# Optimization experiments

Measured on AMD Instinct MI355X. Metric: run time of the kernel, lower is better.

## Reference

```python
import jax, jax.numpy as jnp
import numpy as np

B_G = 16        # number of point clouds
N_PER = 32768   # points per cloud (equal -> no padding)
T = B_G * N_PER
CIN = 16
D = 32          # global_dim
H = 4           # num_heads
HD = D // H
L = 2           # layers
EPS_LN = 1e-5
EPS_Z = 1e-6


def setup_inputs() -> dict:
    key = jax.random.key(0)
    ks = jax.random.split(key, 32)
    r = lambda i, shape, s: (jax.random.normal(ks[i], shape, dtype=jnp.float32) * s)
    inp = {
        "x": r(0, (T, CIN), 1.0),
        "pos": r(1, (T, 3), 1.0),
        "batch": (jnp.arange(T, dtype=jnp.int32) // N_PER),
        "w_in": r(2, (CIN, D), CIN ** -0.5),
        "b_in": r(3, (D,), 0.02),
        "w_pos": r(4, (3, D), 3 ** -0.5),
        "b_pos": r(5, (D,), 0.02),
        "wq": r(6, (L, D, D), D ** -0.5),
        "bq": r(7, (L, D), 0.02),
        "wk": r(8, (L, D, D), D ** -0.5),
        "bk": r(9, (L, D), 0.02),
        "wv": r(10, (L, D, D), D ** -0.5),
        "bv": r(11, (L, D), 0.02),
        "wo": r(12, (L, D, D), D ** -0.5),
        "bo": r(13, (L, D), 0.02),
        "g1": jnp.ones((L, D), jnp.float32),
        "be1": jnp.zeros((L, D), jnp.float32),
        "w1": r(14, (L, D, 2 * D), D ** -0.5),
        "bf1": r(15, (L, 2 * D), 0.02),
        "w2": r(16, (L, 2 * D, D), (2 * D) ** -0.5),
        "bf2": r(17, (L, D), 0.02),
        "g2": jnp.ones((L, D), jnp.float32),
        "be2": jnp.zeros((L, D), jnp.float32),
    }
    return inp


def _layernorm(h, g, b):
    mu = jnp.mean(h, axis=-1, keepdims=True)
    var = jnp.mean(jnp.square(h - mu), axis=-1, keepdims=True)
    return (h - mu) * jax.lax.rsqrt(var + EPS_LN) * g + b


def _linear_attn(h, wq, bq, wk, bk, wv, bv, wo, bo):
    B, N, C = h.shape
    def heads(w, b):
        return (h @ w + b).reshape(B, N, H, HD).transpose(0, 2, 1, 3)  # [B,H,N,hd]
    q = jax.nn.elu(heads(wq, bq)) + 1.0   # ELU feature map phi(.)
    k = jax.nn.elu(heads(wk, bk)) + 1.0
    v = heads(wv, bv)
    kv = jnp.einsum("bhnd,bhne->bhde", k, v)            # O(N) KV summary
    ksum = k.sum(axis=2)                                   # [B,H,hd]
    z = 1.0 / (jnp.einsum("bhnd,bhd->bhn", q, ksum) + EPS_Z)
    out = jnp.einsum("bhnd,bhde->bhne", q, kv) * z[..., None]
    out = out.transpose(0, 2, 1, 3).reshape(B, N, C)
    return out @ wo + bo


def reference(x, pos, batch, w_in, b_in, w_pos, b_pos, wq, bq, wk, bk, wv, bv,
              wo, bo, g1, be1, w1, bf1, w2, bf2, g2, be2):
    # to_dense_batch: batch is sorted; compute per-point index within its segment
    counts = jax.ops.segment_sum(jnp.ones((T,), jnp.int32), batch, num_segments=B_G)
    starts = jnp.concatenate([jnp.zeros((1,), jnp.int32), jnp.cumsum(counts)[:-1]])
    idx = jnp.arange(T, dtype=jnp.int32) - starts[batch]
    x_dense = jnp.zeros((B_G, N_PER, CIN), x.dtype).at[batch, idx].set(x)
    pos_dense = jnp.zeros((B_G, N_PER, 3), pos.dtype).at[batch, idx].set(pos)

    h = (x_dense @ w_in + b_in) + (pos_dense @ w_pos + b_pos)  # [B,N,D]
    for l in range(L):
        h = _layernorm(h + _linear_attn(h, wq[l], bq[l], wk[l], bk[l],
                                        wv[l], bv[l], wo[l], bo[l]), g1[l], be1[l])
        ffn = jax.nn.relu(h @ w1[l] + bf1[l]) @ w2[l] + bf2[l]
        h = _layernorm(h + ffn, g2[l], be2[l])
    return h[batch, idx]  # back to [T, D] (h[mask])
```

## Files before the change

### kernel.cpp

```cpp
#include <hip/hip_runtime.h>

#define KVSZ 288
#define EPS_LN 1e-5f
#define EPS_Z  1e-6f

typedef __attribute__((ext_vector_type(8))) short bf16x8;
typedef __attribute__((ext_vector_type(4))) float f32x4;

#define MFMA(a, b, c) __builtin_amdgcn_mfma_f32_16x16x32_bf16(a, b, c, 0, 0, 0)

#define WQ  0
#define WO  1024
#define KVM 2048
#define W1  3072
#define W2  5120
#define WKN 7168
#define WVN 8192

__device__ __forceinline__ unsigned short f2bf(float f) {
  union { float f; unsigned u; } x; x.f = f;
  unsigned r = x.u + 0x7fff + ((x.u >> 16) & 1);
  return (unsigned short)(r >> 16);
}

__device__ __forceinline__ unsigned pkbf(float a, float b) {
#if __has_builtin(__builtin_amdgcn_cvt_pk_bf16_f32)
  typedef __attribute__((ext_vector_type(2))) __bf16 bf16x2_t;
  bf16x2_t v = __builtin_amdgcn_cvt_pk_bf16_f32(a, b);
  return __builtin_bit_cast(unsigned, v);
#else
  return (unsigned)f2bf(a) | ((unsigned)f2bf(b) << 16);
#endif
}

__device__ __forceinline__ void lds_fence() { asm volatile("s_waitcnt lgkmcnt(0)" ::: "memory"); }
__device__ __forceinline__ float phi(float x) { return x > 0.f ? x + 1.f : __expf(x); }

__device__ __forceinline__ int perm32(int kp) {
  return ((kp & 4) << 2) | (((kp >> 3) << 2) + (kp & 3));
}

__device__ __forceinline__ bf16x8 bbuild(f32x4 lo, f32x4 hi) {
  union { bf16x8 v; unsigned u[4]; } cv;
  cv.u[0] = pkbf(lo[0], lo[1]); cv.u[1] = pkbf(lo[2], lo[3]);
  cv.u[2] = pkbf(hi[0], hi[1]); cv.u[3] = pkbf(hi[2], hi[3]);
  return cv.v;
}

__device__ __forceinline__ void stage_a32(unsigned short* dst, const float* __restrict__ W,
                                          int N, int tid) {
  for (int i = tid; i < 32 * N; i += 256) {
    int n = i >> 5, kp = i & 31;
    dst[i] = f2bf(W[perm32(kp) * N + n]);
  }
}
__device__ __forceinline__ void stage_a64(unsigned short* dst, const float* __restrict__ W,
                                          int tid) {
  for (int i = tid; i < 64 * 32; i += 256) {
    int n = i >> 6, kp = i & 63;
    int kl = ((kp >> 5) << 5) + perm32(kp & 31);
    dst[i] = f2bf(W[kl * 32 + n]);
  }
}
__device__ __forceinline__ void stage_kvm_t(unsigned short* dst, const float* __restrict__ kvg,
                                            int tid) {
  for (int i = tid; i < 1024; i += 256) {
    int e = i >> 5, kp = i & 31;
    int d = perm32(kp);
    float v = ((d >> 3) == (e >> 3)) ? kvg[(e >> 3) * 64 + (d & 7) * 8 + (e & 7)] : 0.f;
    dst[i] = f2bf(v);
  }
}

__device__ __forceinline__ void ln_t(f32x4& a0, f32x4& a1, float4 g0, float4 g1,
                                     float4 b0, float4 b1) {
  float s = a0[0] + a0[1] + a0[2] + a0[3] + a1[0] + a1[1] + a1[2] + a1[3];
  s += __shfl_xor(s, 16); s += __shfl_xor(s, 32);
  float mu = s * (1.f / 32.f);
  float vv = 0.f;
#pragma unroll
  for (int r = 0; r < 4; r++) {
    a0[r] -= mu; a1[r] -= mu;
    vv += a0[r] * a0[r] + a1[r] * a1[r];
  }
  vv += __shfl_xor(vv, 16); vv += __shfl_xor(vv, 32);
  float rstd = rsqrtf(vv * (1.f / 32.f) + EPS_LN);
  a0[0] = a0[0] * rstd * g0.x + b0.x; a0[1] = a0[1] * rstd * g0.y + b0.y;
  a0[2] = a0[2] * rstd * g0.z + b0.z; a0[3] = a0[3] * rstd * g0.w + b0.w;
  a1[0] = a1[0] * rstd * g1.x + b1.x; a1[1] = a1[1] * rstd * g1.y + b1.y;
  a1[2] = a1[2] * rstd * g1.z + b1.z; a1[3] = a1[3] * rstd * g1.w + b1.w;
}

__device__ __forceinline__ void layer_core_t(
    f32x4* hc0, f32x4* hc1, const unsigned short* ws, int quad, int m,
    const float* __restrict__ bq, const float* __restrict__ bo,
    const float* __restrict__ g1, const float* __restrict__ be1,
    const float* __restrict__ bf1, const float* __restrict__ bf2,
    const float* __restrict__ g2, const float* __restrict__ be2,
    const float* __restrict__ kvg) {
  const int k0 = quad * 8, q4 = quad * 4;
  {
    const bf16x8 wqA0 = *(const bf16x8*)(ws + WQ + m * 32 + k0);
    const bf16x8 wqA1 = *(const bf16x8*)(ws + WQ + (16 + m) * 32 + k0);
    const bf16x8 kvA0 = *(const bf16x8*)(ws + KVM + m * 32 + k0);
    const bf16x8 kvA1 = *(const bf16x8*)(ws + KVM + (16 + m) * 32 + k0);
    const bf16x8 woA0 = *(const bf16x8*)(ws + WO + m * 32 + k0);
    const bf16x8 woA1 = *(const bf16x8*)(ws + WO + (16 + m) * 32 + k0);
    const float4 bq0 = *(const float4*)(bq + q4), bq1 = *(const float4*)(bq + 16 + q4);
    const float4 bo0 = *(const float4*)(bo + q4), bo1 = *(const float4*)(bo + 16 + q4);
    const float4 g10 = *(const float4*)(g1 + q4), g11 = *(const float4*)(g1 + 16 + q4);
    const float4 e10 = *(const float4*)(be1 + q4), e11 = *(const float4*)(be1 + 16 + q4);
    const float4 ks0 = *(const float4*)(kvg + 256 + q4);
    const float4 ks1 = *(const float4*)(kvg + 272 + q4);
#pragma unroll
    for (int mt = 0; mt < 4; mt++) {
      bf16x8 hB = bbuild(hc0[mt], hc1[mt]);
      f32x4 q0 = {bq0.x, bq0.y, bq0.z, bq0.w};
      f32x4 q1 = {bq1.x, bq1.y, bq1.z, bq1.w};
      q0 = MFMA(wqA0, hB, q0);
      q1 = MFMA(wqA1, hB, q1);
#pragma unroll
      for (int r = 0; r < 4; r++) { q0[r] = phi(q0[r]); q1[r] = phi(q1[r]); }
      bf16x8 qB = bbuild(q0, q1);
      f32x4 zz = {0.f, 0.f, 0.f, 0.f};
      f32x4 at0 = MFMA(kvA0, qB, zz);
      f32x4 at1 = MFMA(kvA1, qB, zz);
      float p0 = q0[0] * ks0.x + q0[1] * ks0.y + q0[2] * ks0.z + q0[3] * ks0.w;
      float p1 = q1[0] * ks1.x + q1[1] * ks1.y + q1[2] * ks1.z + q1[3] * ks1.w;
      p0 += __shfl_xor(p0, 16);
      p1 += __shfl_xor(p1, 16);
      float z0 = 1.f / (p0 + EPS_Z), z1 = 1.f / (p1 + EPS_Z);
      bf16x8 aB;
      {
        union { bf16x8 v; unsigned u[4]; } cv;
        cv.u[0] = pkbf(at0[0] * z0, at0[1] * z0); cv.u[1] = pkbf(at0[2] * z0, at0[3] * z0);
        cv.u[2] = pkbf(at1[0] * z1, at1[1] * z1); cv.u[3] = pkbf(at1[2] * z1, at1[3] * z1);
        aB = cv.v;
      }
      f32x4 h0 = hc0[mt], h1 = hc1[mt];
      h0[0] += bo0.x; h0[1] += bo0.y; h0[2] += bo0.z; h0[3] += bo0.w;
      h1[0] += bo1.x; h1[1] += bo1.y; h1[2] += bo1.z; h1[3] += bo1.w;
      h0 = MFMA(woA0, aB, h0);
      h1 = MFMA(woA1, aB, h1);
      ln_t(h0, h1, g10, g11, e10, e11);
      hc0[mt] = h0; hc1[mt] = h1;
    }
  }
  {
    bf16x8 w1A[4]; float4 b1f[4];
#pragma unroll
    for (int nt = 0; nt < 4; nt++) {
      w1A[nt] = *(const bf16x8*)(ws + W1 + (nt * 16 + m) * 32 + k0);
      b1f[nt] = *(const float4*)(bf1 + nt * 16 + q4);
    }
    const bf16x8 w2L0 = *(const bf16x8*)(ws + W2 + m * 64 + k0);
    const bf16x8 w2H0 = *(const bf16x8*)(ws + W2 + m * 64 + 32 + k0);
    const bf16x8 w2L1 = *(const bf16x8*)(ws + W2 + (16 + m) * 64 + k0);
    const bf16x8 w2H1 = *(const bf16x8*)(ws + W2 + (16 + m) * 64 + 32 + k0);
    const float4 b20 = *(const float4*)(bf2 + q4), b21 = *(const float4*)(bf2 + 16 + q4);
    const float4 g20 = *(const float4*)(g2 + q4), g21 = *(const float4*)(g2 + 16 + q4);
    const float4 e20 = *(const float4*)(be2 + q4), e21 = *(const float4*)(be2 + 16 + q4);
#pragma unroll
    for (int mt = 0; mt < 4; mt++) {
      bf16x8 hB = bbuild(hc0[mt], hc1[mt]);
      f32x4 hd[4];
#pragma unroll
      for (int nt = 0; nt < 4; nt++) {
        f32x4 ini = {b1f[nt].x, b1f[nt].y, b1f[nt].z, b1f[nt].w};
        hd[nt] = MFMA(w1A[nt], hB, ini);
#pragma unroll
        for (int r = 0; r < 4; r++) hd[nt][r] = fmaxf(hd[nt][r], 0.f);
      }
      bf16x8 fL = bbuild(hd[0], hd[1]);
      bf16x8 fH = bbuild(hd[2], hd[3]);
      f32x4 o0 = hc0[mt], o1 = hc1[mt];
      o0[0] += b20.x; o0[1] += b20.y; o0[2] += b20.z; o0[3] += b20.w;
      o1[0] += b21.x; o1[1] += b21.y; o1[2] += b21.z; o1[3] += b21.w;
      o0 = MFMA(w2L0, fL, o0);
      o0 = MFMA(w2H0, fH, o0);
      o1 = MFMA(w2L1, fL, o1);
      o1 = MFMA(w2H1, fH, o1);
      ln_t(o0, o1, g20, g21, e20, e21);
      hc0[mt] = o0; hc1[mt] = o1;
    }
  }
}

__device__ __forceinline__ void kv_stage_t(
    const f32x4* hc0, const f32x4* hc1, unsigned short* tw, const unsigned short* ws,
    int offk, int offv, float* blk, int quad, int m,
    const float* __restrict__ bk, const float* __restrict__ bv) {
  const int k0 = quad * 8, q4 = quad * 4;
  unsigned short* Tk = tw;
  unsigned short* Tv = tw + 1280;
  const bf16x8 wkA0 = *(const bf16x8*)(ws + offk + m * 32 + k0);
  const bf16x8 wkA1 = *(const bf16x8*)(ws + offk + (16 + m) * 32 + k0);
  const bf16x8 wvA0 = *(const bf16x8*)(ws + offv + m * 32 + k0);
  const bf16x8 wvA1 = *(const bf16x8*)(ws + offv + (16 + m) * 32 + k0);
  const float4 bk0 = *(const float4*)(bk + q4), bk1 = *(const float4*)(bk + 16 + q4);
  const float4 bv0 = *(const float4*)(bv + q4), bv1 = *(const float4*)(bv + 16 + q4);
  f32x4 accA = {0.f, 0.f, 0.f, 0.f}, accB = {0.f, 0.f, 0.f, 0.f};
  f32x4 ksa0 = {0.f, 0.f, 0.f, 0.f}, ksa1 = {0.f, 0.f, 0.f, 0.f};
#pragma unroll
  for (int ch = 0; ch < 2; ch++) {
#pragma unroll
    for (int mtl = 0; mtl < 2; mtl++) {
      int mt = ch * 2 + mtl;
      bf16x8 hB = bbuild(hc0[mt], hc1[mt]);
      f32x4 kn0 = {bk0.x, bk0.y, bk0.z, bk0.w};
      f32x4 kn1 = {bk1.x, bk1.y, bk1.z, bk1.w};
      f32x4 vn0 = {bv0.x, bv0.y, bv0.z, bv0.w};
      f32x4 vn1 = {bv1.x, bv1.y, bv1.z, bv1.w};
      kn0 = MFMA(wkA0, hB, kn0);
      kn1 = MFMA(wkA1, hB, kn1);
      vn0 = MFMA(wvA0, hB, vn0);
      vn1 = MFMA(wvA1, hB, vn1);
      int cb = mtl * 16 + m;
#pragma unroll
      for (int r = 0; r < 4; r++) {
        kn0[r] = phi(kn0[r]); kn1[r] = phi(kn1[r]);
        ksa0[r] += kn0[r];    ksa1[r] += kn1[r];
        Tk[(q4 + r) * 40 + cb]      = f2bf(kn0[r]);
        Tk[(16 + q4 + r) * 40 + cb] = f2bf(kn1[r]);
        Tv[(q4 + r) * 40 + cb]      = f2bf(vn0[r]);
        Tv[(16 + q4 + r) * 40 + cb] = f2bf(vn1[r]);
      }
    }
    lds_fence();
    bf16x8 akL = *(const bf16x8*)(Tk + m * 40 + k0);
    bf16x8 akH = *(const bf16x8*)(Tk + (16 + m) * 40 + k0);
    bf16x8 avL = *(const bf16x8*)(Tv + m * 40 + k0);
    bf16x8 avH = *(const bf16x8*)(Tv + (16 + m) * 40 + k0);
    accA = MFMA(akL, avL, accA);
    accB = MFMA(akH, avH, accB);
    lds_fence();
  }
#pragma unroll
  for (int r = 0; r < 4; r++) {
    float v0 = ksa0[r], v1 = ksa1[r];
    v0 += __shfl_xor(v0, 1); v0 += __shfl_xor(v0, 2); v0 += __shfl_xor(v0, 4); v0 += __shfl_xor(v0, 8);
    v1 += __shfl_xor(v1, 1); v1 += __shfl_xor(v1, 2); v1 += __shfl_xor(v1, 4); v1 += __shfl_xor(v1, 8);
    if (m == 0) {
      atomicAdd(&blk[256 + q4 + r], v0);
      atomicAdd(&blk[272 + q4 + r], v1);
    }
  }
  if ((quad >> 1) == (m >> 3)) {
    int h0 = quad >> 1, h1 = 2 + (quad >> 1), e = m & 7;
#pragma unroll
    for (int r = 0; r < 4; r++) {
      int d = (q4 + r) & 7;
      atomicAdd(&blk[h0 * 64 + d * 8 + e], accA[r]);
      atomicAdd(&blk[h1 * 64 + d * 8 + e], accB[r]);
    }
  }
}

__global__ __launch_bounds__(256) void k_embed(
    const float* __restrict__ x, const float* __restrict__ pos,
    const float* __restrict__ w_in, const float* __restrict__ b_in,
    const float* __restrict__ w_pos, const float* __restrict__ b_pos,
    const float* __restrict__ wk, const float* __restrict__ bk,
    const float* __restrict__ wv, const float* __restrict__ bv,
    float* __restrict__ hout, float* __restrict__ gkv) {
  __shared__ __align__(16) unsigned short ws[3072];
  __shared__ __align__(16) unsigned short tiles[4 * 2560];
  __shared__ float blk[KVSZ];
  const int tid = threadIdx.x;
  const int wv_ = tid >> 6, lane = tid & 63, quad = lane >> 4, m = lane & 15;
  unsigned short* tw = tiles + wv_ * 2560;
  for (int i = tid; i < 1024; i += 256) {
    int n = i >> 5, k = i & 31;
    float v = k < 16 ? w_in[k * 32 + n] : (k < 19 ? w_pos[(k - 16) * 32 + n] : 0.f);
    ws[i] = f2bf(v);
  }
  stage_a32(ws + 1024, wk, 32, tid);
  stage_a32(ws + 2048, wv, 32, tid);
  for (int i = tid; i < KVSZ; i += 256) blk[i] = 0.f;
  __syncthreads();
  const int wbase = blockIdx.x * 256 + wv_ * 64;
  const int cloud = blockIdx.x >> 7;
  const int k0 = quad * 8, q4 = quad * 4;
  const bf16x8 weA0 = *(const bf16x8*)(ws + m * 32 + k0);
  const bf16x8 weA1 = *(const bf16x8*)(ws + (16 + m) * 32 + k0);
  float4 bi0, bi1;
  {
    float4 a = *(const float4*)(b_in + q4), b = *(const float4*)(b_pos + q4);
    bi0 = make_float4(a.x + b.x, a.y + b.y, a.z + b.z, a.w + b.w);
    float4 c = *(const float4*)(b_in + 16 + q4), d = *(const float4*)(b_pos + 16 + q4);
    bi1 = make_float4(c.x + d.x, c.y + d.y, c.z + d.z, c.w + d.w);
  }
  f32x4 hc0[4], hc1[4];
#pragma unroll
  for (int mt = 0; mt < 4; mt++) {
    int p = wbase + mt * 16 + m;
    union { bf16x8 v; unsigned u[4]; } xb;
    xb.u[0] = xb.u[1] = xb.u[2] = xb.u[3] = 0;
    if (quad < 2) {
      const float4* xp = (const float4*)(x + (size_t)p * 16 + quad * 8);
      float4 t0 = xp[0], t1 = xp[1];
      xb.u[0] = pkbf(t0.x, t0.y); xb.u[1] = pkbf(t0.z, t0.w);
      xb.u[2] = pkbf(t1.x, t1.y); xb.u[3] = pkbf(t1.z, t1.w);
    } else if (quad == 2) {
      const float* pp = pos + (size_t)p * 3;
      xb.u[0] = pkbf(pp[0], pp[1]); xb.u[1] = pkbf(pp[2], 0.f);
    }
    f32x4 i0 = {bi0.x, bi0.y, bi0.z, bi0.w};
    f32x4 i1 = {bi1.x, bi1.y, bi1.z, bi1.w};
    hc0[mt] = MFMA(weA0, xb.v, i0);
    hc1[mt] = MFMA(weA1, xb.v, i1);
    float* hp = hout + (size_t)p * 32;
    *(float4*)(hp + q4)      = make_float4(hc0[mt][0], hc0[mt][1], hc0[mt][2], hc0[mt][3]);
    *(float4*)(hp + 16 + q4) = make_float4(hc1[mt][0], hc1[mt][1], hc1[mt][2], hc1[mt][3]);
  }
  kv_stage_t(hc0, hc1, tw, ws, 1024, 2048, blk, quad, m, bk, bv);
  __syncthreads();
  float* g = gkv + cloud * KVSZ;
  for (int i = tid; i < KVSZ; i += 256) atomicAdd(&g[i], blk[i]);
}

__global__ __launch_bounds__(256) void k_mid(
    const float* __restrict__ wq, const float* __restrict__ bq,
    const float* __restrict__ wo, const float* __restrict__ bo,
    const float* __restrict__ g1, const float* __restrict__ be1,
    const float* __restrict__ w1, const float* __restrict__ bf1,
    const float* __restrict__ w2, const float* __restrict__ bf2,
    const float* __restrict__ g2, const float* __restrict__ be2,
    const float* __restrict__ wkn, const float* __restrict__ bkn,
    const float* __restrict__ wvn, const float* __restrict__ bvn,
    const float* __restrict__ kv_in, float* __restrict__ gkv_out,
    float* __restrict__ hbuf) {
  __shared__ __align__(16) unsigned short ws[9216];
  __shared__ __align__(16) unsigned short tiles[4 * 2560];
  __shared__ float blk[KVSZ];
  const int tid = threadIdx.x;
  const int wv_ = tid >> 6, lane = tid & 63, quad = lane >> 4, m = lane & 15;
  unsigned short* tw = tiles + wv_ * 2560;
  const int cloud = blockIdx.x >> 7;
  stage_a32(ws + WQ, wq, 32, tid);
  stage_a32(ws + WO, wo, 32, tid);
  stage_kvm_t(ws + KVM, kv_in + cloud * KVSZ, tid);
  stage_a32(ws + W1, w1, 64, tid);
  stage_a64(ws + W2, w2, tid);
  stage_a32(ws + WKN, wkn, 32, tid);
  stage_a32(ws + WVN, wvn, 32, tid);
  for (int i = tid; i < KVSZ; i += 256) blk[i] = 0.f;
  __syncthreads();
  const int wbase = blockIdx.x * 256 + wv_ * 64;
  const int q4 = quad * 4;
  f32x4 hc0[4], hc1[4];
#pragma unroll
  for (int mt = 0; mt < 4; mt++) {
    const float* hp = hbuf + (size_t)(wbase + mt * 16 + m) * 32;
    float4 lo = *(const float4*)(hp + q4);
    float4 hi = *(const float4*)(hp + 16 + q4);
    hc0[mt][0] = lo.x; hc0[mt][1] = lo.y; hc0[mt][2] = lo.z; hc0[mt][3] = lo.w;
    hc1[mt][0] = hi.x; hc1[mt][1] = hi.y; hc1[mt][2] = hi.z; hc1[mt][3] = hi.w;
  }
  layer_core_t(hc0, hc1, ws, quad, m, bq, bo, g1, be1, bf1, bf2, g2, be2,
               kv_in + cloud * KVSZ);
#pragma unroll
  for (int mt = 0; mt < 4; mt++) {
    float* hp = hbuf + (size_t)(wbase + mt * 16 + m) * 32;
    *(float4*)(hp + q4)      = make_float4(hc0[mt][0], hc0[mt][1], hc0[mt][2], hc0[mt][3]);
    *(float4*)(hp + 16 + q4) = make_float4(hc1[mt][0], hc1[mt][1], hc1[mt][2], hc1[mt][3]);
  }
  kv_stage_t(hc0, hc1, tw, ws, WKN, WVN, blk, quad, m, bkn, bvn);
  __syncthreads();
  float* g = gkv_out + cloud * KVSZ;
  for (int i = tid; i < KVSZ; i += 256) atomicAdd(&g[i], blk[i]);
}

__global__ __launch_bounds__(256) void k_last(
    const float* __restrict__ wq, const float* __restrict__ bq,
    const float* __restrict__ wo, const float* __restrict__ bo,
    const float* __restrict__ g1, const float* __restrict__ be1,
    const float* __restrict__ w1, const float* __restrict__ bf1,
    const float* __restrict__ w2, const float* __restrict__ bf2,
    const float* __restrict__ g2, const float* __restrict__ be2,
    const float* __restrict__ kv_in, float* __restrict__ hbuf) {
  __shared__ __align__(16) unsigned short ws[7168];
  const int tid = threadIdx.x;
  const int wv_ = tid >> 6, lane = tid & 63, quad = lane >> 4, m = lane & 15;
  const int cloud = blockIdx.x >> 7;
  stage_a32(ws + WQ, wq, 32, tid);
  stage_a32(ws + WO, wo, 32, tid);
  stage_kvm_t(ws + KVM, kv_in + cloud * KVSZ, tid);
  stage_a32(ws + W1, w1, 64, tid);
  stage_a64(ws + W2, w2, tid);
  __syncthreads();
  const int wbase = blockIdx.x * 256 + wv_ * 64;
  const int q4 = quad * 4;
  f32x4 hc0[4], hc1[4];
#pragma unroll
  for (int mt = 0; mt < 4; mt++) {
    const float* hp = hbuf + (size_t)(wbase + mt * 16 + m) * 32;
    float4 lo = *(const float4*)(hp + q4);
    float4 hi = *(const float4*)(hp + 16 + q4);
    hc0[mt][0] = lo.x; hc0[mt][1] = lo.y; hc0[mt][2] = lo.z; hc0[mt][3] = lo.w;
    hc1[mt][0] = hi.x; hc1[mt][1] = hi.y; hc1[mt][2] = hi.z; hc1[mt][3] = hi.w;
  }
  layer_core_t(hc0, hc1, ws, quad, m, bq, bo, g1, be1, bf1, bf2, g2, be2,
               kv_in + cloud * KVSZ);
#pragma unroll
  for (int mt = 0; mt < 4; mt++) {
    float* hp = hbuf + (size_t)(wbase + mt * 16 + m) * 32;
    *(float4*)(hp + q4)      = make_float4(hc0[mt][0], hc0[mt][1], hc0[mt][2], hc0[mt][3]);
    *(float4*)(hp + 16 + q4) = make_float4(hc1[mt][0], hc1[mt][1], hc1[mt][2], hc1[mt][3]);
  }
}

extern "C" void kernel_launch(void* const* d_in, const int* in_sizes, int n_in,
                              void* d_out, int out_size, void* d_ws, size_t ws_size,
                              hipStream_t stream) {
  (void)in_sizes; (void)n_in; (void)out_size; (void)ws_size;
  const float* x     = (const float*)d_in[0];
  const float* pos   = (const float*)d_in[1];
  const float* w_in  = (const float*)d_in[3];
  const float* b_in  = (const float*)d_in[4];
  const float* w_pos = (const float*)d_in[5];
  const float* b_pos = (const float*)d_in[6];
  const float* wq  = (const float*)d_in[7];
  const float* bq  = (const float*)d_in[8];
  const float* wk  = (const float*)d_in[9];
  const float* bk  = (const float*)d_in[10];
  const float* wv  = (const float*)d_in[11];
  const float* bv  = (const float*)d_in[12];
  const float* wo  = (const float*)d_in[13];
  const float* bo  = (const float*)d_in[14];
  const float* g1  = (const float*)d_in[15];
  const float* be1 = (const float*)d_in[16];
  const float* w1  = (const float*)d_in[17];
  const float* bf1 = (const float*)d_in[18];
  const float* w2  = (const float*)d_in[19];
  const float* bf2 = (const float*)d_in[20];
  const float* g2  = (const float*)d_in[21];
  const float* be2 = (const float*)d_in[22];
  float* out   = (float*)d_out;
  float* kvbuf = (float*)d_ws;

  hipMemsetAsync(kvbuf, 0, 2 * 16 * KVSZ * sizeof(float), stream);
  dim3 grid(2048), block(256);
  k_embed<<<grid, block, 0, stream>>>(x, pos, w_in, b_in, w_pos, b_pos,
                                      wk, bk, wv, bv, out, kvbuf);
  k_mid<<<grid, block, 0, stream>>>(wq, bq, wo, bo, g1, be1, w1, bf1, w2, bf2, g2, be2,
                                    wk + 1024, bk + 32, wv + 1024, bv + 32,
                                    kvbuf, kvbuf + 16 * KVSZ, out);
  k_last<<<grid, block, 0, stream>>>(wq + 1024, bq + 32, wo + 1024, bo + 32,
                                     g1 + 32, be1 + 32, w1 + 2048, bf1 + 64,
                                     w2 + 2048, bf2 + 32, g2 + 32, be2 + 32,
                                     kvbuf + 16 * KVSZ, out);
}
```

Measured before the change: 306.9 us.

## Prepack bf16 weights once, build KV matrix in registers, store activations as bf16

A single-block prep kernel now converts and permutes all weights to bf16 in workspace once. The main kernels read these A-fragments straight from global memory, so they no longer redo per-block LDS staging and its barrier. The block-diagonal KV matrix is assembled per lane in registers instead of in LDS. When the workspace is large enough, the intermediate hidden state between kernels is kept in bf16 instead of fp32, halving that traffic at some cost in precision. The trade-off is an extra serial launch and global-memory weight reads.

```diff
diff --git a/kernel.cpp b/kernel.cpp
--- a/kernel.cpp
+++ b/kernel.cpp
@@ -9,13 +9,14 @@
 
 #define MFMA(a, b, c) __builtin_amdgcn_mfma_f32_16x16x32_bf16(a, b, c, 0, 0, 0)
 
-#define WQ  0
-#define WO  1024
-#define KVM 2048
-#define W1  3072
-#define W2  5120
-#define WKN 7168
-#define WVN 8192
+#define PWE 0
+#define LBASE(l) (1024 + (l) * 8192)
+#define PQ 0
+#define PO 1024
+#define P1 2048
+#define P2 4096
+#define PK 6144
+#define PV 7168
 
 __device__ __forceinline__ unsigned short f2bf(float f) {
   union { float f; unsigned u; } x; x.f = f;
@@ -33,6 +34,10 @@
 #endif
 }
 
+__device__ __forceinline__ float bfu(unsigned short s) {
+  union { float f; unsigned u; } x; x.u = ((unsigned)s) << 16; return x.f;
+}
+
 __device__ __forceinline__ void lds_fence() { asm volatile("s_waitcnt lgkmcnt(0)" ::: "memory"); }
 __device__ __forceinline__ float phi(float x) { return x > 0.f ? x + 1.f : __expf(x); }
 
@@ -62,14 +67,23 @@
     dst[i] = f2bf(W[kl * 32 + n]);
   }
 }
-__device__ __forceinline__ void stage_kvm_t(unsigned short* dst, const float* __restrict__ kvg,
-                                            int tid) {
-  for (int i = tid; i < 1024; i += 256) {
-    int e = i >> 5, kp = i & 31;
-    int d = perm32(kp);
-    float v = ((d >> 3) == (e >> 3)) ? kvg[(e >> 3) * 64 + (d & 7) * 8 + (e & 7)] : 0.f;
-    dst[i] = f2bf(v);
-  }
+
+__device__ __forceinline__ void make_kvm(bf16x8& A0, bf16x8& A1,
+                                         const float* __restrict__ kvg,
+                                         int quad, int m) {
+  union { bf16x8 v; unsigned short s[8]; unsigned u[4]; } a, b;
+  a.u[0] = a.u[1] = a.u[2] = a.u[3] = 0u;
+  b.u[0] = b.u[1] = b.u[2] = b.u[3] = 0u;
+  if ((quad >> 1) == (m >> 3)) {
+    int h0 = m >> 3, e7 = m & 7, dq = (quad & 1) * 4;
+    const float* p0 = kvg + h0 * 64 + dq * 8 + e7;
+    const float* p1 = kvg + (2 + h0) * 64 + dq * 8 + e7;
+    a.s[0] = f2bf(p0[0]);  a.s[1] = f2bf(p0[8]);
+    a.s[2] = f2bf(p0[16]); a.s[3] = f2bf(p0[24]);
+    b.s[4] = f2bf(p1[0]);  b.s[5] = f2bf(p1[8]);
+    b.s[6] = f2bf(p1[16]); b.s[7] = f2bf(p1[24]);
+  }
+  A0 = a.v; A1 = b.v;
 }
 
 __device__ __forceinline__ void ln_t(f32x4& a0, f32x4& a1, float4 g0, float4 g1,
@@ -91,21 +105,21 @@
   a1[2] = a1[2] * rstd * g1.z + b1.z; a1[3] = a1[3] * rstd * g1.w + b1.w;
 }
 
-__device__ __forceinline__ void layer_core_t(
-    f32x4* hc0, f32x4* hc1, const unsigned short* ws, int quad, int m,
+__device__ __forceinline__ void layer_core_g(
+    f32x4 (&hc0)[4], f32x4 (&hc1)[4], const unsigned short* __restrict__ pwl,
+    const float* __restrict__ kvg, int quad, int m,
     const float* __restrict__ bq, const float* __restrict__ bo,
     const float* __restrict__ g1, const float* __restrict__ be1,
     const float* __restrict__ bf1, const float* __restrict__ bf2,
-    const float* __restrict__ g2, const float* __restrict__ be2,
-    const float* __restrict__ kvg) {
+    const float* __restrict__ g2, const float* __restrict__ be2) {
   const int k0 = quad * 8, q4 = quad * 4;
   {
-    const bf16x8 wqA0 = *(const bf16x8*)(ws + WQ + m * 32 + k0);
-    const bf16x8 wqA1 = *(const bf16x8*)(ws + WQ + (16 + m) * 32 + k0);
-    const bf16x8 kvA0 = *(const bf16x8*)(ws + KVM + m * 32 + k0);
-    const bf16x8 kvA1 = *(const bf16x8*)(ws + KVM + (16 + m) * 32 + k0);
-    const bf16x8 woA0 = *(const bf16x8*)(ws + WO + m * 32 + k0);
-    const bf16x8 woA1 = *(const bf16x8*)(ws + WO + (16 + m) * 32 + k0);
+    const bf16x8 wqA0 = *(const bf16x8*)(pwl + PQ + m * 32 + k0);
+    const bf16x8 wqA1 = *(const bf16x8*)(pwl + PQ + (16 + m) * 32 + k0);
+    const bf16x8 woA0 = *(const bf16x8*)(pwl + PO + m * 32 + k0);
+    const bf16x8 woA1 = *(const bf16x8*)(pwl + PO + (16 + m) * 32 + k0);
+    bf16x8 kvA0, kvA1;
+    make_kvm(kvA0, kvA1, kvg, quad, m);
     const float4 bq0 = *(const float4*)(bq + q4), bq1 = *(const float4*)(bq + 16 + q4);
     const float4 bo0 = *(const float4*)(bo + q4), bo1 = *(const float4*)(bo + 16 + q4);
     const float4 g10 = *(const float4*)(g1 + q4), g11 = *(const float4*)(g1 + 16 + q4);
@@ -150,13 +164,13 @@
     bf16x8 w1A[4]; float4 b1f[4];
 #pragma unroll
     for (int nt = 0; nt < 4; nt++) {
-      w1A[nt] = *(const bf16x8*)(ws + W1 + (nt * 16 + m) * 32 + k0);
+      w1A[nt] = *(const bf16x8*)(pwl + P1 + (nt * 16 + m) * 32 + k0);
       b1f[nt] = *(const float4*)(bf1 + nt * 16 + q4);
     }
-    const bf16x8 w2L0 = *(const bf16x8*)(ws + W2 + m * 64 + k0);
-    const bf16x8 w2H0 = *(const bf16x8*)(ws + W2 + m * 64 + 32 + k0);
-    const bf16x8 w2L1 = *(const bf16x8*)(ws + W2 + (16 + m) * 64 + k0);
-    const bf16x8 w2H1 = *(const bf16x8*)(ws + W2 + (16 + m) * 64 + 32 + k0);
+    const bf16x8 w2L0 = *(const bf16x8*)(pwl + P2 + m * 64 + k0);
+    const bf16x8 w2H0 = *(const bf16x8*)(pwl + P2 + m * 64 + 32 + k0);
+    const bf16x8 w2L1 = *(const bf16x8*)(pwl + P2 + (16 + m) * 64 + k0);
+    const bf16x8 w2H1 = *(const bf16x8*)(pwl + P2 + (16 + m) * 64 + 32 + k0);
     const float4 b20 = *(const float4*)(bf2 + q4), b21 = *(const float4*)(bf2 + 16 + q4);
     const float4 g20 = *(const float4*)(g2 + q4), g21 = *(const float4*)(g2 + 16 + q4);
     const float4 e20 = *(const float4*)(be2 + q4), e21 = *(const float4*)(be2 + 16 + q4);
@@ -186,17 +200,18 @@
   }
 }
 
-__device__ __forceinline__ void kv_stage_t(
-    const f32x4* hc0, const f32x4* hc1, unsigned short* tw, const unsigned short* ws,
-    int offk, int offv, float* blk, int quad, int m,
+__device__ __forceinline__ void kv_stage_g(
+    const f32x4 (&hc0)[4], const f32x4 (&hc1)[4], unsigned short* tw,
+    const unsigned short* __restrict__ pwk, const unsigned short* __restrict__ pwv,
+    float* blk, int quad, int m,
     const float* __restrict__ bk, const float* __restrict__ bv) {
   const int k0 = quad * 8, q4 = quad * 4;
   unsigned short* Tk = tw;
   unsigned short* Tv = tw + 1280;
-  const bf16x8 wkA0 = *(const bf16x8*)(ws + offk + m * 32 + k0);
-  const bf16x8 wkA1 = *(const bf16x8*)(ws + offk + (16 + m) * 32 + k0);
-  const bf16x8 wvA0 = *(const bf16x8*)(ws + offv + m * 32 + k0);
-  const bf16x8 wvA1 = *(const bf16x8*)(ws + offv + (16 + m) * 32 + k0);
+  const bf16x8 wkA0 = *(const bf16x8*)(pwk + m * 32 + k0);
+  const bf16x8 wkA1 = *(const bf16x8*)(pwk + (16 + m) * 32 + k0);
+  const bf16x8 wvA0 = *(const bf16x8*)(pwv + m * 32 + k0);
+  const bf16x8 wvA1 = *(const bf16x8*)(pwv + (16 + m) * 32 + k0);
   const float4 bk0 = *(const float4*)(bk + q4), bk1 = *(const float4*)(bk + 16 + q4);
   const float4 bv0 = *(const float4*)(bv + q4), bv1 = *(const float4*)(bv + 16 + q4);
   f32x4 accA = {0.f, 0.f, 0.f, 0.f}, accB = {0.f, 0.f, 0.f, 0.f};
@@ -256,33 +271,48 @@
   }
 }
 
+__global__ __launch_bounds__(256) void k_prep(
+    const float* __restrict__ w_in, const float* __restrict__ w_pos,
+    const float* __restrict__ wq, const float* __restrict__ wk,
+    const float* __restrict__ wv, const float* __restrict__ wo,
+    const float* __restrict__ w1, const float* __restrict__ w2,
+    unsigned short* __restrict__ pw) {
+  const int tid = threadIdx.x;
+  for (int i = tid; i < 1024; i += 256) {
+    int n = i >> 5, k = i & 31;
+    float v = k < 16 ? w_in[k * 32 + n] : (k < 19 ? w_pos[(k - 16) * 32 + n] : 0.f);
+    pw[PWE + i] = f2bf(v);
+  }
+  for (int l = 0; l < 2; l++) {
+    unsigned short* b = pw + LBASE(l);
+    stage_a32(b + PQ, wq + l * 1024, 32, tid);
+    stage_a32(b + PO, wo + l * 1024, 32, tid);
+    stage_a32(b + P1, w1 + l * 2048, 64, tid);
+    stage_a64(b + P2, w2 + l * 2048, tid);
+    stage_a32(b + PK, wk + l * 1024, 32, tid);
+    stage_a32(b + PV, wv + l * 1024, 32, tid);
+  }
+}
+
+template <int H16>
 __global__ __launch_bounds__(256) void k_embed(
     const float* __restrict__ x, const float* __restrict__ pos,
-    const float* __restrict__ w_in, const float* __restrict__ b_in,
-    const float* __restrict__ w_pos, const float* __restrict__ b_pos,
-    const float* __restrict__ wk, const float* __restrict__ bk,
-    const float* __restrict__ wv, const float* __restrict__ bv,
-    float* __restrict__ hout, float* __restrict__ gkv) {
-  __shared__ __align__(16) unsigned short ws[3072];
+    const float* __restrict__ b_in, const float* __restrict__ b_pos,
+    const float* __restrict__ bk, const float* __restrict__ bv,
+    const unsigned short* __restrict__ pw, unsigned short* __restrict__ hb,
+    float* __restrict__ hf, float* __restrict__ gkv) {
   __shared__ __align__(16) unsigned short tiles[4 * 2560];
   __shared__ float blk[KVSZ];
   const int tid = threadIdx.x;
   const int wv_ = tid >> 6, lane = tid & 63, quad = lane >> 4, m = lane & 15;
   unsigned short* tw = tiles + wv_ * 2560;
-  for (int i = tid; i < 1024; i += 256) {
-    int n = i >> 5, k = i & 31;
-    float v = k < 16 ? w_in[k * 32 + n] : (k < 19 ? w_pos[(k - 16) * 32 + n] : 0.f);
-    ws[i] = f2bf(v);
-  }
-  stage_a32(ws + 1024, wk, 32, tid);
-  stage_a32(ws + 2048, wv, 32, tid);
+  const int cloud = blockIdx.x >> 7;
+  const int wbase = blockIdx.x * 256 + wv_ * 64;
+  const int k0 = quad * 8, q4 = quad * 4;
   for (int i = tid; i < KVSZ; i += 256) blk[i] = 0.f;
   __syncthreads();
-  const int wbase = blockIdx.x * 256 + wv_ * 64;
-  const int cloud = blockIdx.x >> 7;
-  const int k0 = quad * 8, q4 = quad * 4;
-  const bf16x8 weA0 = *(const bf16x8*)(ws + m * 32 + k0);
-  const bf16x8 weA1 = *(const bf16x8*)(ws + (16 + m) * 32 + k0);
+  const bf16x8 weA0 = *(const bf16x8*)(pw + PWE + m * 32 + k0);
+  const bf16x8 weA1 = *(const bf16x8*)(pw + PWE + (16 + m) * 32 + k0);
   float4 bi0, bi1;
   {
     float4 a = *(const float4*)(b_in + q4), b = *(const float4*)(b_pos + q4);
@@ -309,102 +339,117 @@
     f32x4 i1 = {bi1.x, bi1.y, bi1.z, bi1.w};
     hc0[mt] = MFMA(weA0, xb.v, i0);
     hc1[mt] = MFMA(weA1, xb.v, i1);
-    float* hp = hout + (size_t)p * 32;
-    *(float4*)(hp + q4)      = make_float4(hc0[mt][0], hc0[mt][1], hc0[mt][2], hc0[mt][3]);
-    *(float4*)(hp + 16 + q4) = make_float4(hc1[mt][0], hc1[mt][1], hc1[mt][2], hc1[mt][3]);
-  }
-  kv_stage_t(hc0, hc1, tw, ws, 1024, 2048, blk, quad, m, bk, bv);
+    if (H16) {
+      *(bf16x8*)(hb + ((size_t)p * 32 + quad * 8)) = bbuild(hc0[mt], hc1[mt]);
+    } else {
+      float* hp = hf + (size_t)p * 32;
+      *(float4*)(hp + q4)      = make_float4(hc0[mt][0], hc0[mt][1], hc0[mt][2], hc0[mt][3]);
+      *(float4*)(hp + 16 + q4) = make_float4(hc1[mt][0], hc1[mt][1], hc1[mt][2], hc1[mt][3]);
+    }
+  }
+  kv_stage_g(hc0, hc1, tw, pw + LBASE(0) + PK, pw + LBASE(0) + PV, blk, quad, m, bk, bv);
   __syncthreads();
   float* g = gkv + cloud * KVSZ;
   for (int i = tid; i < KVSZ; i += 256) atomicAdd(&g[i], blk[i]);
 }
 
+template <int H16>
 __global__ __launch_bounds__(256) void k_mid(
-    const float* __restrict__ wq, const float* __restrict__ bq,
-    const float* __restrict__ wo, const float* __restrict__ bo,
+    const float* __restrict__ bq, const float* __restrict__ bo,
     const float* __restrict__ g1, const float* __restrict__ be1,
-    const float* __restrict__ w1, const float* __restrict__ bf1,
-    const float* __restrict__ w2, const float* __restrict__ bf2,
+    const float* __restrict__ bf1, const float* __restrict__ bf2,
     const float* __restrict__ g2, const float* __restrict__ be2,
-    const float* __restrict__ wkn, const float* __restrict__ bkn,
-    const float* __restrict__ wvn, const float* __restrict__ bvn,
-    const float* __restrict__ kv_in, float* __restrict__ gkv_out,
-    float* __restrict__ hbuf) {
-  __shared__ __align__(16) unsigned short ws[9216];
+    const float* __restrict__ bkn, const float* __restrict__ bvn,
+    const unsigned short* __restrict__ pw, const float* __restrict__ kv_in,
+    float* __restrict__ gkv_out, unsigned short* __restrict__ hb,
+    float* __restrict__ hf) {
   __shared__ __align__(16) unsigned short tiles[4 * 2560];
   __shared__ float blk[KVSZ];
   const int tid = threadIdx.x;
   const int wv_ = tid >> 6, lane = tid & 63, quad = lane >> 4, m = lane & 15;
   unsigned short* tw = tiles + wv_ * 2560;
   const int cloud = blockIdx.x >> 7;
-  stage_a32(ws + WQ, wq, 32, tid);
-  stage_a32(ws + WO, wo, 32, tid);
-  stage_kvm_t(ws + KVM, kv_in + cloud * KVSZ, tid);
-  stage_a32(ws + W1, w1, 64, tid);
-  stage_a64(ws + W2, w2, tid);
-  stage_a32(ws + WKN, wkn, 32, tid);
-  stage_a32(ws + WVN, wvn, 32, tid);
+  const int wbase = blockIdx.x * 256 + wv_ * 64;
+  const int q4 = quad * 4;
   for (int i = tid; i < KVSZ; i += 256) blk[i] = 0.f;
   __syncthreads();
+  f32x4 hc0[4], hc1[4];
+#pragma unroll
+  for (int mt = 0; mt < 4; mt++) {
+    int p = wbase + mt * 16 + m;
+    if (H16) {
+      bf16x8 hv = *(const bf16x8*)(hb + ((size_t)p * 32 + quad * 8));
+#pragma unroll
+      for (int r = 0; r < 4; r++) {
+        hc0[mt][r] = bfu((unsigned short)hv[r]);
+        hc1[mt][r] = bfu((unsigned short)hv[4 + r]);
+      }
+    } else {
+      const float* hp = hf + (size_t)p * 32;
+      float4 lo = *(const float4*)(hp + q4);
+      float4 hi = *(const float4*)(hp + 16 + q4);
+      hc0[mt][0] = lo.x; hc0[mt][1] = lo.y; hc0[mt][2] = lo.z; hc0[mt][3] = lo.w;
+      hc1[mt][0] = hi.x; hc1[mt][1] = hi.y; hc1[mt][2] = hi.z; hc1[mt][3] = hi.w;
+    }
+  }
+  layer_core_g(hc0, hc1, pw + LBASE(0), kv_in + cloud * KVSZ, quad, m,
+               bq, bo, g1, be1, bf1, bf2, g2, be2);
+#pragma unroll
+  for (int mt = 0; mt < 4; mt++) {
+    int p = wbase + mt * 16 + m;
+    if (H16) {
+      *(bf16x8*)(hb + ((size_t)p * 32 + quad * 8)) = bbuild(hc0[mt], hc1[mt]);
+    } else {
+      float* hp = hf + (size_t)p * 32;
+      *(float4*)(hp + q4)      = make_float4(hc0[mt][0], hc0[mt][1], hc0[mt][2], hc0[mt][3]);
+      *(float4*)(hp + 16 + q4) = make_float4(hc1[mt][0], hc1[mt][1], hc1[mt][2], hc1[mt][3]);
+    }
+  }
+  kv_stage_g(hc0, hc1, tw, pw + LBASE(1) + PK, pw + LBASE(1) + PV, blk, quad, m,
+             bkn, bvn);
+  __syncthreads();
+  float* g = gkv_out + cloud * KVSZ;
+  for (int i = tid; i < KVSZ; i += 256) atomicAdd(&g[i], blk[i]);
+}
+
+template <int H16>
+__global__ __launch_bounds__(256) void k_last(
+    const float* __restrict__ bq, const float* __restrict__ bo,
+    const float* __restrict__ g1, const float* __restrict__ be1,
+    const float* __restrict__ bf1, const float* __restrict__ bf2,
+    const float* __restrict__ g2, const float* __restrict__ be2,
+    const unsigned short* __restrict__ pw, const float* __restrict__ kv_in,
+    const unsigned short* __restrict__ hb, float* __restrict__ out) {
+  const int tid = threadIdx.x;
+  const int wv_ = tid >> 6, lane = tid & 63, quad = lane >> 4, m = lane & 15;
+  const int cloud = blockIdx.x >> 7;
   const int wbase = blockIdx.x * 256 + wv_ * 64;
   const int q4 = quad * 4;
   f32x4 hc0[4], hc1[4];
 #pragma unroll
   for (int mt = 0; mt < 4; mt++) {
-    const float* hp = hbuf + (size_t)(wbase + mt * 16 + m) * 32;
-    float4 lo = *(const float4*)(hp + q4);
-    float4 hi = *(const float4*)(hp + 16 + q4);
-    hc0[mt][0] = lo.x; hc0[mt][1] = lo.y; hc0[mt][2] = lo.z; hc0[mt][3] = lo.w;
-    hc1[mt][0] = hi.x; hc1[mt][1] = hi.y; hc1[mt][2] = hi.z; hc1[mt][3] = hi.w;
-  }
-  layer_core_t(hc0, hc1, ws, quad, m, bq, bo, g1, be1, bf1, bf2, g2, be2,
-               kv_in + cloud * KVSZ);
+    int p = wbase + mt * 16 + m;
+    if (H16) {
+      bf16x8 hv = *(const bf16x8*)(hb + ((size_t)p * 32 + quad * 8));
+#pragma unroll
+      for (int r = 0; r < 4; r++) {
+        hc0[mt][r] = bfu((unsigned short)hv[r]);
+        hc1[mt][r] = bfu((unsigned short)hv[4 + r]);
+      }
+    } else {
+      const float* hp = out + (size_t)p * 32;
+      float4 lo = *(const float4*)(hp + q4);
+      float4 hi = *(const float4*)(hp + 16 + q4);
+      hc0[mt][0] = lo.x; hc0[mt][1] = lo.y; hc0[mt][2] = lo.z; hc0[mt][3] = lo.w;
+      hc1[mt][0] = hi.x; hc1[mt][1] = hi.y; hc1[mt][2] = hi.z; hc1[mt][3] = hi.w;
+    }
+  }
+  layer_core_g(hc0, hc1, pw + LBASE(1), kv_in + cloud * KVSZ, quad, m,
+               bq, bo, g1, be1, bf1, bf2, g2, be2);
 #pragma unroll
   for (int mt = 0; mt < 4; mt++) {
-    float* hp = hbuf + (size_t)(wbase + mt * 16 + m) * 32;
-    *(float4*)(hp + q4)      = make_float4(hc0[mt][0], hc0[mt][1], hc0[mt][2], hc0[mt][3]);
-    *(float4*)(hp + 16 + q4) = make_float4(hc1[mt][0], hc1[mt][1], hc1[mt][2], hc1[mt][3]);
-  }
-  kv_stage_t(hc0, hc1, tw, ws, WKN, WVN, blk, quad, m, bkn, bvn);
-  __syncthreads();
-  float* g = gkv_out + cloud * KVSZ;
-  for (int i = tid; i < KVSZ; i += 256) atomicAdd(&g[i], blk[i]);
-}
-
-__global__ __launch_bounds__(256) void k_last(
-    const float* __restrict__ wq, const float* __restrict__ bq,
-    const float* __restrict__ wo, const float* __restrict__ bo,
-    const float* __restrict__ g1, const float* __restrict__ be1,
-    const float* __restrict__ w1, const float* __restrict__ bf1,
-    const float* __restrict__ w2, const float* __restrict__ bf2,
-    const float* __restrict__ g2, const float* __restrict__ be2,
-    const float* __restrict__ kv_in, float* __restrict__ hbuf) {
-  __shared__ __align__(16) unsigned short ws[7168];
-  const int tid = threadIdx.x;
-  const int wv_ = tid >> 6, lane = tid & 63, quad = lane >> 4, m = lane & 15;
-  const int cloud = blockIdx.x >> 7;
-  stage_a32(ws + WQ, wq, 32, tid);
-  stage_a32(ws + WO, wo, 32, tid);
-  stage_kvm_t(ws + KVM, kv_in + cloud * KVSZ, tid);
-  stage_a32(ws + W1, w1, 64, tid);
-  stage_a64(ws + W2, w2, tid);
-  __syncthreads();
-  const int wbase = blockIdx.x * 256 + wv_ * 64;
-  const int q4 = quad * 4;
-  f32x4 hc0[4], hc1[4];
-#pragma unroll
-  for (int mt = 0; mt < 4; mt++) {
-    const float* hp = hbuf + (size_t)(wbase + mt * 16 + m) * 32;
-    float4 lo = *(const float4*)(hp + q4);
-    float4 hi = *(const float4*)(hp + 16 + q4);
-    hc0[mt][0] = lo.x; hc0[mt][1] = lo.y; hc0[mt][2] = lo.z; hc0[mt][3] = lo.w;
-    hc1[mt][0] = hi.x; hc1[mt][1] = hi.y; hc1[mt][2] = hi.z; hc1[mt][3] = hi.w;
-  }
-  layer_core_t(hc0, hc1, ws, quad, m, bq, bo, g1, be1, bf1, bf2, g2, be2,
-               kv_in + cloud * KVSZ);
-#pragma unroll
-  for (int mt = 0; mt < 4; mt++) {
-    float* hp = hbuf + (size_t)(wbase + mt * 16 + m) * 32;
+    int p = wbase + mt * 16 + m;
+    float* hp = out + (size_t)p * 32;
     *(float4*)(hp + q4)      = make_float4(hc0[mt][0], hc0[mt][1], hc0[mt][2], hc0[mt][3]);
     *(float4*)(hp + 16 + q4) = make_float4(hc1[mt][0], hc1[mt][1], hc1[mt][2], hc1[mt][3]);
   }
@@ -413,7 +458,7 @@
 extern "C" void kernel_launch(void* const* d_in, const int* in_sizes, int n_in,
                               void* d_out, int out_size, void* d_ws, size_t ws_size,
                               hipStream_t stream) {
-  (void)in_sizes; (void)n_in; (void)out_size; (void)ws_size;
+  (void)in_sizes; (void)n_in; (void)out_size;
   const float* x     = (const float*)d_in[0];
   const float* pos   = (const float*)d_in[1];
   const float* w_in  = (const float*)d_in[3];
@@ -436,18 +481,31 @@
   const float* bf2 = (const float*)d_in[20];
   const float* g2  = (const float*)d_in[21];
   const float* be2 = (const float*)d_in[22];
-  float* out   = (float*)d_out;
+  float* out = (float*)d_out;
   float* kvbuf = (float*)d_ws;
+  unsigned short* pw = (unsigned short*)((char*)d_ws + 40960);
+  unsigned short* hb = (unsigned short*)((char*)d_ws + 131072);
+  const size_t need = 131072ull + 524288ull * 32ull * 2ull;
+  const bool h16 = ws_size >= need;
 
   hipMemsetAsync(kvbuf, 0, 2 * 16 * KVSZ * sizeof(float), stream);
+  k_prep<<<dim3(1), dim3(256), 0, stream>>>(w_in, w_pos, wq, wk, wv, wo, w1, w2, pw);
   dim3 grid(2048), block(256);
-  k_embed<<<grid, block, 0, stream>>>(x, pos, w_in, b_in, w_pos, b_pos,
-                                      wk, bk, wv, bv, out, kvbuf);
-  k_mid<<<grid, block, 0, stream>>>(wq, bq, wo, bo, g1, be1, w1, bf1, w2, bf2, g2, be2,
-                                    wk + 1024, bk + 32, wv + 1024, bv + 32,
-                                    kvbuf, kvbuf + 16 * KVSZ, out);
-  k_last<<<grid, block, 0, stream>>>(wq + 1024, bq + 32, wo + 1024, bo + 32,
-                                     g1 + 32, be1 + 32, w1 + 2048, bf1 + 64,
-                                     w2 + 2048, bf2 + 32, g2 + 32, be2 + 32,
-                                     kvbuf + 16 * KVSZ, out);
-}
+  if (h16) {
+    k_embed<1><<<grid, block, 0, stream>>>(x, pos, b_in, b_pos, bk, bv, pw, hb, out, kvbuf);
+    k_mid<1><<<grid, block, 0, stream>>>(bq, bo, g1, be1, bf1, bf2, g2, be2,
+                                         bk + 32, bv + 32, pw, kvbuf,
+                                         kvbuf + 16 * KVSZ, hb, out);
+    k_last<1><<<grid, block, 0, stream>>>(bq + 32, bo + 32, g1 + 32, be1 + 32,
+                                          bf1 + 64, bf2 + 32, g2 + 32, be2 + 32,
+                                          pw, kvbuf + 16 * KVSZ, hb, out);
+  } else {
+    k_embed<0><<<grid, block, 0, stream>>>(x, pos, b_in, b_pos, bk, bv, pw, hb, out, kvbuf);
+    k_mid<0><<<grid, block, 0, stream>>>(bq, bo, g1, be1, bf1, bf2, g2, be2,
+                                         bk + 32, bv + 32, pw, kvbuf,
+                                         kvbuf + 16 * KVSZ, hb, out);
+    k_last<0><<<grid, block, 0, stream>>>(bq + 32, bo + 32, g1 + 32, be1 + 32,
+                                          bf1 + 64, bf2 + 32, g2 + 32, be2 + 32,
+                                          pw, kvbuf + 16 * KVSZ, hb, out);
+  }
+}
```

Result: faster. 267.2 us (-13.0%).
